# Performance work log

Measured on AMD Instinct MI355X. Metric: run time of the kernel, lower is better.

## Reference

```python
import jax, jax.numpy as jnp
import numpy as np

B, S, E, H, SHARE = 32, 1024, 256, 256, 2


def setup_inputs() -> dict:
    key = jax.random.key(0)
    ks = jax.random.split(key, 14)
    sc_e = 1.0 / np.sqrt(E)
    sc_h = 1.0 / np.sqrt(H)
    mk = lambda k, shape, sc: (jax.random.normal(k, shape, jnp.float32) * sc)
    return {
        "inputs": jax.random.normal(ks[0], (B, S, E), jnp.float32),
        "mask": jnp.ones((B, S), jnp.float32),
        # forward-direction cell params
        "Wx": mk(ks[1], (E, 4 * H), sc_e),
        "Wh": mk(ks[2], (H, 4 * H), sc_h),
        "Ws": mk(ks[3], (H, 4 * H), sc_h),
        "b": jnp.zeros((4 * H,), jnp.float32),
        "Wrx": mk(ks[4], (SHARE, E, H), sc_e),
        "Wrh": mk(ks[5], (SHARE, H, H), sc_h),
        "br": jnp.zeros((SHARE, H), jnp.float32),
        # reverse-direction cell params (deepcopy in torch; distinct draws here)
        "Wx_r": mk(ks[6], (E, 4 * H), sc_e),
        "Wh_r": mk(ks[7], (H, 4 * H), sc_h),
        "Ws_r": mk(ks[8], (H, 4 * H), sc_h),
        "b_r": jnp.zeros((4 * H,), jnp.float32),
        "Wrx_r": mk(ks[9], (SHARE, E, H), sc_e),
        "Wrh_r": mk(ks[10], (SHARE, H, H), sc_h),
        "br_r": jnp.zeros((SHARE, H), jnp.float32),
        "idx": 1,
    }


def _run_dir(xs, ms, params, idx, reverse):
    # xs: [S,B,E] time-major, ms: [S,B]
    Wx, Wh, Ws, b, Wrx, Wrh, br = params
    if reverse:
        xs = xs[::-1]
        ms = ms[::-1]
    Bt = xs.shape[1]
    Hd = Wh.shape[0]
    K = Wrx.shape[0]
    h0 = jnp.zeros((Bt, Hd), xs.dtype)
    c0 = jnp.zeros((Bt, Hd), xs.dtype)
    s0 = jnp.zeros((K, Bt, Hd), xs.dtype)  # shared cells (init_s)

    def step(carry, xm):
        h, c, s = carry
        x_t, m_t = xm
        # gates read x, h, and the idx-selected shared cell
        z = x_t @ Wx + h @ Wh + s[idx] @ Ws + b  # [B, 4H]
        i, f, g, o = jnp.split(z, 4, axis=-1)
        c_new = jax.nn.sigmoid(f) * c + jax.nn.sigmoid(i) * jnp.tanh(g)
        h_new = jax.nn.sigmoid(o) * jnp.tanh(c_new)
        m = m_t[:, None]
        h = m * h_new + (1.0 - m) * h
        c = m * c_new + (1.0 - m) * c
        # shared-cell gates, all K at once: [K,B,H]
        r = jax.nn.sigmoid(
            jnp.einsum("be,keh->kbh", x_t, Wrx)
            + jnp.einsum("bh,khj->kbj", h, Wrh)
            + br[:, None, :]
        )
        s_new = r * s + (1.0 - r) * c[None]
        s = m[None] * s_new + (1.0 - m[None]) * s
        return (h, c, s), (h, c, s)

    _, (hs, cs, ss) = jax.lax.scan(step, (h0, c0, s0), (xs, ms))
    if reverse:
        hs, cs, ss = hs[::-1], cs[::-1], ss[::-1]
    return hs, cs, ss  # [S,B,H], [S,B,H], [S,K,B,H]


def reference(inputs, mask, Wx, Wh, Ws, b, Wrx, Wrh, br,
              Wx_r, Wh_r, Ws_r, b_r, Wrx_r, Wrh_r, br_r, idx):
    xs = inputs.transpose(1, 0, 2)  # [S,B,E]
    ms = mask.T  # [S,B]
    hs_f, cs_f, ss_f = _run_dir(xs, ms, (Wx, Wh, Ws, b, Wrx, Wrh, br), idx, False)
    hs_r, cs_r, ss_r = _run_dir(xs, ms, (Wx_r, Wh_r, Ws_r, b_r, Wrx_r, Wrh_r, br_r), idx, True)
    h_f = jnp.concatenate([hs_f, hs_r], axis=-1)  # [S,B,2H]
    c_f = jnp.concatenate([cs_f, cs_r], axis=-1)  # [S,B,2H]
    # final_list: per shared-cell index, stacked over time -> [K,S,B,2H]
    s_f = jnp.concatenate([ss_f, ss_r], axis=-1).transpose(1, 0, 2, 3)
    return (h_f, c_f, s_f)
```

## Files before the change

### kernel.cpp

```cpp
#include <hip/hip_runtime.h>
#include <hip/hip_bf16.h>
#include <cstdint>
#include <cstddef>


typedef __bf16 bf16x8 __attribute__((ext_vector_type(8)));
typedef float  f32x4  __attribute__((ext_vector_type(4)));

#define DEVINL __device__ __forceinline__

constexpr int Bb = 32, Ss = 1024;
constexpr int NWG = 32;

constexpr size_t OFF_CTR = 0;
constexpr size_t OFF_H   = 1024;
constexpr size_t SZ_HS   = (size_t)2*2*32*256*2;
constexpr size_t OFF_S   = OFF_H + SZ_HS;
constexpr size_t OFF_WX  = OFF_S + SZ_HS;
constexpr size_t SZ_W    = (size_t)2*1024*256*2;
constexpr size_t OFF_WS  = OFF_WX + SZ_W;
constexpr size_t OFF_WRX = OFF_WS + SZ_W;
constexpr size_t SZ_WR   = (size_t)2*2*256*256*2;
constexpr size_t OFF_WRH = OFF_WRX + SZ_WR;

DEVINL unsigned short f2bf(float f) {
    unsigned u = __builtin_bit_cast(unsigned, f);
    u += 0x7FFFu + ((u >> 16) & 1u);
    return (unsigned short)(u >> 16);
}
DEVINL float sigm(float x) { return 1.f / (1.f + __expf(-x)); }

__global__ void prepass(const float* __restrict__ Wx0, const float* __restrict__ Ws0,
                        const float* __restrict__ Wx1, const float* __restrict__ Ws1,
                        const float* __restrict__ Wrx0, const float* __restrict__ Wrh0,
                        const float* __restrict__ Wrx1, const float* __restrict__ Wrh1,
                        unsigned char* __restrict__ ws)
{
    unsigned short* wxT  = (unsigned short*)(ws + OFF_WX);
    unsigned short* wsT  = (unsigned short*)(ws + OFF_WS);
    unsigned short* wrxT = (unsigned short*)(ws + OFF_WRX);
    unsigned short* wrhT = (unsigned short*)(ws + OFF_WRH);
    int tid = blockIdx.x * blockDim.x + threadIdx.x;
    int NT  = gridDim.x * blockDim.x;
    for (int e = tid; e < 2*1024*256; e += NT) {
        int d = e >> 18, r = e & 262143, n = r >> 8, k = r & 255;
        const float* wx = d ? Wx1 : Wx0;
        const float* wz = d ? Ws1 : Ws0;
        wxT[e] = f2bf(wx[k*1024 + n]);
        wsT[e] = f2bf(wz[k*1024 + n]);
    }
    for (int e = tid; e < 2*2*256*256; e += NT) {
        int d = e >> 17, r = e & 131071, kk = r >> 16, r2 = r & 65535;
        int j = r2 >> 8, k = r2 & 255;
        const float* wrx = d ? Wrx1 : Wrx0;
        const float* wrh = d ? Wrh1 : Wrh0;
        wrxT[e] = f2bf(wrx[(kk*256 + k)*256 + j]);
        wrhT[e] = f2bf(wrh[(kk*256 + k)*256 + j]);
    }
    unsigned* z = (unsigned*)(ws + OFF_H);
    for (int e = tid; e < (int)(2*SZ_HS/4); e += NT) z[e] = 0u;
    if (tid < 256) ((unsigned*)ws)[tid] = 0u;
}

__launch_bounds__(256, 1)
__global__ void bislstm(const float* __restrict__ inputs, const float* __restrict__ mask,
                        const float* __restrict__ Wh0, const float* __restrict__ Wh1,
                        const float* __restrict__ b0,  const float* __restrict__ b1,
                        const float* __restrict__ br0, const float* __restrict__ br1,
                        const int* __restrict__ idxp,
                        unsigned char* __restrict__ ws, float* __restrict__ out)
{
    const int bid = blockIdx.x;
    const int d   = bid >> 5;
    const int g   = bid & 31;
    const int tid = threadIdx.x;
    const int wave = tid >> 6, lane = tid & 63;
    const int lm = lane & 15, lq = lane >> 4;

    __shared__ __align__(16) unsigned short sWh[32][264];
    __shared__ __align__(16) unsigned short sA[32][520];
    __shared__ float zs[2][32][16];
    __shared__ float rsx[32][16], rsh[32][16];
    __shared__ float sC[32][8], sH[32][8], sS[2][32][8];
    __shared__ unsigned short sHb[256], sSb[256];

    const float* Whd = d ? Wh1 : Wh0;
    const float* bd  = d ? b1  : b0;
    const float* brd = d ? br1 : br0;
    const unsigned short* wxT  = (const unsigned short*)(ws + OFF_WX)  + (size_t)d*1024*256;
    const unsigned short* wsT  = (const unsigned short*)(ws + OFF_WS)  + (size_t)d*1024*256;
    const unsigned short* wrxT = (const unsigned short*)(ws + OFF_WRX) + (size_t)d*2*256*256;
    const unsigned short* wrhT = (const unsigned short*)(ws + OFF_WRH) + (size_t)d*2*256*256;
    unsigned long long* Hbuf = (unsigned long long*)(ws + OFF_H);
    unsigned long long* Sbuf = (unsigned long long*)(ws + OFF_S);
    unsigned* ctr = (unsigned*)(ws + OFF_CTR) + (size_t)d*64;
    const int idxv = idxp[0];

    for (int i = 0; i < 32; ++i) {
        int e = tid + 256*i, k = e >> 5, nl = e & 31;
        int col = (nl >> 3)*256 + g*8 + (nl & 7);
        sWh[nl][k] = f2bf(Whd[(size_t)k*1024 + col]);
    }
    {
        int b_ = tid >> 3, j = tid & 7;
        sC[b_][j] = 0.f; sH[b_][j] = 0.f; sS[0][b_][j] = 0.f; sS[1][b_][j] = 0.f;
    }
    __syncthreads();

    const int eb = tid >> 3, ej = tid & 7;
    const int gj = g*8 + ej;
    const float bias_i = bd[gj], bias_f = bd[256+gj], bias_g = bd[512+gj], bias_o = bd[768+gj];
    const float brr0 = brd[gj], brr1 = brd[256+gj];

    const int zMt = wave & 1, zNt = wave >> 1;
    const int znl = zNt*16 + lm;
    const int zcol = (znl >> 3)*256 + g*8 + (znl & 7);
    const int rMt = wave & 1;
    const int rks = lm >> 3;
    const int rj  = g*8 + (lm & 7);

    unsigned tgt = 0;
#define GRID_BARRIER()                                                          \
    do {                                                                        \
        __syncthreads();                                                        \
        if (tid == 0) {                                                         \
            __hip_atomic_fetch_add(ctr, 1u, __ATOMIC_RELEASE,                   \
                                   __HIP_MEMORY_SCOPE_AGENT);                   \
            while (__hip_atomic_load(ctr, __ATOMIC_RELAXED,                     \
                                     __HIP_MEMORY_SCOPE_AGENT) < tgt)           \
                __builtin_amdgcn_s_sleep(1);                                    \
            (void)__hip_atomic_load(ctr, __ATOMIC_ACQUIRE,                      \
                                    __HIP_MEMORY_SCOPE_AGENT);                  \
        }                                                                       \
        __syncthreads();                                                        \
    } while (0)

    for (int t = 0; t < Ss; ++t) {
        const int tx = d ? (Ss - 1 - t) : t;
        const int pp = (t + 1) & 1;
        const int pc = t & 1;

        {
            const unsigned long long* hsrc = Hbuf + (size_t)(pp*2 + d)*2048;
            const unsigned long long* ssrc = Sbuf + (size_t)(pp*2 + d)*2048;
#pragma unroll
            for (int i = 0; i < 8; ++i) {
                int e = tid + 256*i;
                int b_ = e >> 6, u4 = e & 63;
                unsigned long long hv = __hip_atomic_load(hsrc + e, __ATOMIC_RELAXED, __HIP_MEMORY_SCOPE_AGENT);
                unsigned long long sv = __hip_atomic_load(ssrc + e, __ATOMIC_RELAXED, __HIP_MEMORY_SCOPE_AGENT);
                *(unsigned long long*)&sA[b_][u4*4]       = hv;
                *(unsigned long long*)&sA[b_][256 + u4*4] = sv;
            }
        }
        __syncthreads();

        f32x4 acc0 = {0.f, 0.f, 0.f, 0.f};
        {
            bf16x8 wsf[8];
#pragma unroll
            for (int kt = 0; kt < 8; ++kt)
                wsf[kt] = *(const bf16x8*)(wsT + (size_t)zcol*256 + 32*kt + 8*lq);
#pragma unroll
            for (int kt = 0; kt < 16; ++kt) {
                bf16x8 a = *(const bf16x8*)&sA[zMt*16 + lm][32*kt + 8*lq];
                bf16x8 bb = (kt < 8) ? *(const bf16x8*)&sWh[znl][32*kt + 8*lq] : wsf[kt - 8];
                acc0 = __builtin_amdgcn_mfma_f32_16x16x32_bf16(a, bb, acc0, 0, 0, 0);
            }
        }
        __syncthreads();

        {
#pragma unroll
            for (int i = 0; i < 8; ++i) {
                int e = tid + 256*i;
                int b_ = e >> 6, c4 = e & 63;
                float4 v = *(const float4*)(inputs + (((size_t)b_*Ss + tx) << 8) + c4*4);
                unsigned long long pk = (unsigned long long)f2bf(v.x)
                                      | ((unsigned long long)f2bf(v.y) << 16)
                                      | ((unsigned long long)f2bf(v.z) << 32)
                                      | ((unsigned long long)f2bf(v.w) << 48);
                *(unsigned long long*)&sA[b_][c4*4] = pk;
            }
        }
        __syncthreads();

        {
            bf16x8 wxf[8];
#pragma unroll
            for (int kt = 0; kt < 8; ++kt)
                wxf[kt] = *(const bf16x8*)(wxT + (size_t)zcol*256 + 32*kt + 8*lq);
#pragma unroll
            for (int kt = 0; kt < 8; ++kt) {
                bf16x8 a = *(const bf16x8*)&sA[zMt*16 + lm][32*kt + 8*lq];
                acc0 = __builtin_amdgcn_mfma_f32_16x16x32_bf16(a, wxf[kt], acc0, 0, 0, 0);
            }
        }
#pragma unroll
        for (int r = 0; r < 4; ++r)
            zs[zNt][zMt*16 + lq*4 + r][lm] = acc0[r];
        __syncthreads();

        float m_, cu_, hu_;
        {
            float zi = zs[0][eb][ej]   + bias_i;
            float zf = zs[0][eb][8+ej] + bias_f;
            float zg = zs[1][eb][ej]   + bias_g;
            float zo = zs[1][eb][8+ej] + bias_o;
            float co = sC[eb][ej], ho = sH[eb][ej];
            float cn = sigm(zf)*co + sigm(zi)*tanhf(zg);
            float hn = sigm(zo)*tanhf(cn);
            m_  = mask[(size_t)eb*Ss + tx];
            cu_ = m_*cn + (1.f - m_)*co;
            hu_ = m_*hn + (1.f - m_)*ho;
            sC[eb][ej] = cu_; sH[eb][ej] = hu_;
            sHb[eb*8 + ej] = f2bf(hu_);
            out[((size_t)tx*32 + eb)*512 + d*256 + gj] = hu_;
            out[16777216 + ((size_t)tx*32 + eb)*512 + d*256 + gj] = cu_;
        }
        __syncthreads();
        if (wave == 0) {
            unsigned long long pk = *(unsigned long long*)&sHb[lane*4];
            int b_ = lane >> 1, half = lane & 1;
            size_t di = (size_t)(pc*2 + d)*2048 + (size_t)b_*64 + g*2 + half;
            __hip_atomic_store(Hbuf + di, pk, __ATOMIC_RELAXED, __HIP_MEMORY_SCOPE_AGENT);
        }
        tgt += NWG; GRID_BARRIER();

        if (wave < 2) {
            f32x4 racc = {0.f, 0.f, 0.f, 0.f};
            bf16x8 wf[8];
#pragma unroll
            for (int kt = 0; kt < 8; ++kt)
                wf[kt] = *(const bf16x8*)(wrxT + (size_t)(rks*256 + rj)*256 + 32*kt + 8*lq);
#pragma unroll
            for (int kt = 0; kt < 8; ++kt) {
                bf16x8 a = *(const bf16x8*)&sA[rMt*16 + lm][32*kt + 8*lq];
                racc = __builtin_amdgcn_mfma_f32_16x16x32_bf16(a, wf[kt], racc, 0, 0, 0);
            }
#pragma unroll
            for (int r = 0; r < 4; ++r)
                rsx[rMt*16 + lq*4 + r][lm] = racc[r];
        }
        __syncthreads();

        {
            const unsigned long long* hsrc = Hbuf + (size_t)(pc*2 + d)*2048;
#pragma unroll
            for (int i = 0; i < 8; ++i) {
                int e = tid + 256*i;
                int b_ = e >> 6, u4 = e & 63;
                unsigned long long hv = __hip_atomic_load(hsrc + e, __ATOMIC_RELAXED, __HIP_MEMORY_SCOPE_AGENT);
                *(unsigned long long*)&sA[b_][256 + u4*4] = hv;
            }
        }
        __syncthreads();

        if (wave >= 2) {
            f32x4 rh = {0.f, 0.f, 0.f, 0.f};
            bf16x8 wf[8];
#pragma unroll
            for (int kt = 0; kt < 8; ++kt)
                wf[kt] = *(const bf16x8*)(wrhT + (size_t)(rks*256 + rj)*256 + 32*kt + 8*lq);
#pragma unroll
            for (int kt = 0; kt < 8; ++kt) {
                bf16x8 a = *(const bf16x8*)&sA[rMt*16 + lm][256 + 32*kt + 8*lq];
                rh = __builtin_amdgcn_mfma_f32_16x16x32_bf16(a, wf[kt], rh, 0, 0, 0);
            }
#pragma unroll
            for (int r = 0; r < 4; ++r)
                rsh[rMt*16 + lq*4 + r][lm] = rh[r];
        }
        __syncthreads();

        {
#pragma unroll
            for (int kk = 0; kk < 2; ++kk) {
                float rv = rsx[eb][kk*8+ej] + rsh[eb][kk*8+ej] + (kk ? brr1 : brr0);
                float rr = sigm(rv);
                float so = sS[kk][eb][ej];
                float sn = rr*so + (1.f - rr)*cu_;
                float su = m_*sn + (1.f - m_)*so;
                sS[kk][eb][ej] = su;
                out[33554432 + (((size_t)kk*1024 + tx)*32 + eb)*512 + d*256 + gj] = su;
                if (kk == idxv) sSb[eb*8 + ej] = f2bf(su);
            }
        }
        __syncthreads();
        if (wave == 0) {
            unsigned long long pk = *(unsigned long long*)&sSb[lane*4];
            int b_ = lane >> 1, half = lane & 1;
            size_t di = (size_t)(pc*2 + d)*2048 + (size_t)b_*64 + g*2 + half;
            __hip_atomic_store(Sbuf + di, pk, __ATOMIC_RELAXED, __HIP_MEMORY_SCOPE_AGENT);
        }
        tgt += NWG; GRID_BARRIER();
    }
#undef GRID_BARRIER
}

extern "C" void kernel_launch(void* const* d_in, const int* in_sizes, int n_in,
                              void* d_out, int out_size, void* d_ws, size_t ws_size,
                              hipStream_t stream) {
    const float* inputs = (const float*)d_in[0];
    const float* mask_  = (const float*)d_in[1];
    const float* Wx0  = (const float*)d_in[2];
    const float* Wh0  = (const float*)d_in[3];
    const float* Ws0  = (const float*)d_in[4];
    const float* b0   = (const float*)d_in[5];
    const float* Wrx0 = (const float*)d_in[6];
    const float* Wrh0 = (const float*)d_in[7];
    const float* br0  = (const float*)d_in[8];
    const float* Wx1  = (const float*)d_in[9];
    const float* Wh1  = (const float*)d_in[10];
    const float* Ws1  = (const float*)d_in[11];
    const float* b1   = (const float*)d_in[12];
    const float* Wrx1 = (const float*)d_in[13];
    const float* Wrh1 = (const float*)d_in[14];
    const float* br1  = (const float*)d_in[15];
    const int*   idxp = (const int*)d_in[16];
    unsigned char* ws = (unsigned char*)d_ws;

    hipLaunchKernelGGL(prepass, dim3(512), dim3(256), 0, stream,
                       Wx0, Ws0, Wx1, Ws1, Wrx0, Wrh0, Wrx1, Wrh1, ws);
    hipLaunchKernelGGL(bislstm, dim3(64), dim3(256), 0, stream,
                       inputs, mask_, Wh0, Wh1, b0, b1, br0, br1, idxp,
                       ws, (float*)d_out);
}
```

Measured before the change: 14.69 ms.

## Replace grid barriers with per-workgroup flags, register-resident weights, prefetch next input

Swaps the counter-based grid barrier for per-workgroup step flags that one wave polls, so each workgroup waits only for data it actually reads. All weight fragments (Wh, Ws, Wx, Wrx/Wrh) are loaded into registers once instead of being re-read from global memory every step. The next timestep's inputs are prefetched into a fragment-ordered shared-memory layout while other waves run, and the per-step sync count drops. This raises register pressure and relies on relaxed atomics plus explicit waitcnt for correctness.

```diff
diff --git a/kernel.cpp b/kernel.cpp
--- a/kernel.cpp
+++ b/kernel.cpp
@@ -6,18 +6,19 @@
 
 typedef __bf16 bf16x8 __attribute__((ext_vector_type(8)));
 typedef float  f32x4  __attribute__((ext_vector_type(4)));
+typedef unsigned long long u64x2 __attribute__((ext_vector_type(2)));
 
 #define DEVINL __device__ __forceinline__
 
-constexpr int Bb = 32, Ss = 1024;
-constexpr int NWG = 32;
-
-constexpr size_t OFF_CTR = 0;
+constexpr int Ss = 1024;
+
+constexpr size_t OFF_FLAGS = 0;
 constexpr size_t OFF_H   = 1024;
-constexpr size_t SZ_HS   = (size_t)2*2*32*256*2;
+constexpr size_t SZ_HS   = (size_t)2*2*32*512;
 constexpr size_t OFF_S   = OFF_H + SZ_HS;
-constexpr size_t OFF_WX  = OFF_S + SZ_HS;
+constexpr size_t OFF_WH  = OFF_S + SZ_HS;
 constexpr size_t SZ_W    = (size_t)2*1024*256*2;
+constexpr size_t OFF_WX  = OFF_WH + SZ_W;
 constexpr size_t OFF_WS  = OFF_WX + SZ_W;
 constexpr size_t OFF_WRX = OFF_WS + SZ_W;
 constexpr size_t SZ_WR   = (size_t)2*2*256*256*2;
@@ -28,14 +29,21 @@
     u += 0x7FFFu + ((u >> 16) & 1u);
     return (unsigned short)(u >> 16);
 }
+DEVINL unsigned long long pack4(float4 v) {
+    return (unsigned long long)f2bf(v.x) | ((unsigned long long)f2bf(v.y) << 16)
+         | ((unsigned long long)f2bf(v.z) << 32) | ((unsigned long long)f2bf(v.w) << 48);
+}
 DEVINL float sigm(float x) { return 1.f / (1.f + __expf(-x)); }
 
-__global__ void prepass(const float* __restrict__ Wx0, const float* __restrict__ Ws0,
-                        const float* __restrict__ Wx1, const float* __restrict__ Ws1,
+__global__ void prepass(const float* __restrict__ Wx0, const float* __restrict__ Wh0,
+                        const float* __restrict__ Ws0,
+                        const float* __restrict__ Wx1, const float* __restrict__ Wh1,
+                        const float* __restrict__ Ws1,
                         const float* __restrict__ Wrx0, const float* __restrict__ Wrh0,
                         const float* __restrict__ Wrx1, const float* __restrict__ Wrh1,
                         unsigned char* __restrict__ ws)
 {
+    unsigned short* whT  = (unsigned short*)(ws + OFF_WH);
     unsigned short* wxT  = (unsigned short*)(ws + OFF_WX);
     unsigned short* wsT  = (unsigned short*)(ws + OFF_WS);
     unsigned short* wrxT = (unsigned short*)(ws + OFF_WRX);
@@ -44,27 +52,24 @@
     int NT  = gridDim.x * blockDim.x;
     for (int e = tid; e < 2*1024*256; e += NT) {
         int d = e >> 18, r = e & 262143, n = r >> 8, k = r & 255;
-        const float* wx = d ? Wx1 : Wx0;
-        const float* wz = d ? Ws1 : Ws0;
-        wxT[e] = f2bf(wx[k*1024 + n]);
-        wsT[e] = f2bf(wz[k*1024 + n]);
+        whT[e] = f2bf((d ? Wh1 : Wh0)[k*1024 + n]);
+        wxT[e] = f2bf((d ? Wx1 : Wx0)[k*1024 + n]);
+        wsT[e] = f2bf((d ? Ws1 : Ws0)[k*1024 + n]);
     }
     for (int e = tid; e < 2*2*256*256; e += NT) {
         int d = e >> 17, r = e & 131071, kk = r >> 16, r2 = r & 65535;
         int j = r2 >> 8, k = r2 & 255;
-        const float* wrx = d ? Wrx1 : Wrx0;
-        const float* wrh = d ? Wrh1 : Wrh0;
-        wrxT[e] = f2bf(wrx[(kk*256 + k)*256 + j]);
-        wrhT[e] = f2bf(wrh[(kk*256 + k)*256 + j]);
-    }
-    unsigned* z = (unsigned*)(ws + OFF_H);
-    for (int e = tid; e < (int)(2*SZ_HS/4); e += NT) z[e] = 0u;
-    if (tid < 256) ((unsigned*)ws)[tid] = 0u;
-}
+        wrxT[e] = f2bf((d ? Wrx1 : Wrx0)[(kk*256 + k)*256 + j]);
+        wrhT[e] = f2bf((d ? Wrh1 : Wrh0)[(kk*256 + k)*256 + j]);
+    }
+    if (blockIdx.x == 0 && threadIdx.x < 256) ((unsigned*)ws)[threadIdx.x] = 0u;
+}
+
+#define FRAG_PTR(Mt,kt,lqv,m) \
+    ((unsigned long long*)(sA + (size_t)(((((Mt)*24+(kt))*4+(lqv))*16+(m))*8)))
 
 __launch_bounds__(256, 1)
 __global__ void bislstm(const float* __restrict__ inputs, const float* __restrict__ mask,
-                        const float* __restrict__ Wh0, const float* __restrict__ Wh1,
                         const float* __restrict__ b0,  const float* __restrict__ b1,
                         const float* __restrict__ br0, const float* __restrict__ br1,
                         const int* __restrict__ idxp,
@@ -77,33 +82,68 @@
     const int wave = tid >> 6, lane = tid & 63;
     const int lm = lane & 15, lq = lane >> 4;
 
-    __shared__ __align__(16) unsigned short sWh[32][264];
-    __shared__ __align__(16) unsigned short sA[32][520];
+    __shared__ __align__(16) unsigned short sA[24576];
     __shared__ float zs[2][32][16];
     __shared__ float rsx[32][16], rsh[32][16];
-    __shared__ float sC[32][8], sH[32][8], sS[2][32][8];
-    __shared__ unsigned short sHb[256], sSb[256];
-
-    const float* Whd = d ? Wh1 : Wh0;
-    const float* bd  = d ? b1  : b0;
-    const float* brd = d ? br1 : br0;
+    __shared__ float sC[32][8], sHs[32][8], sS2[2][32][8];
+    __shared__ __align__(8) unsigned short sHb[256], sSb[256];
+
+    const unsigned short* whT  = (const unsigned short*)(ws + OFF_WH)  + (size_t)d*1024*256;
     const unsigned short* wxT  = (const unsigned short*)(ws + OFF_WX)  + (size_t)d*1024*256;
     const unsigned short* wsT  = (const unsigned short*)(ws + OFF_WS)  + (size_t)d*1024*256;
     const unsigned short* wrxT = (const unsigned short*)(ws + OFF_WRX) + (size_t)d*2*256*256;
     const unsigned short* wrhT = (const unsigned short*)(ws + OFF_WRH) + (size_t)d*2*256*256;
     unsigned long long* Hbuf = (unsigned long long*)(ws + OFF_H);
     unsigned long long* Sbuf = (unsigned long long*)(ws + OFF_S);
-    unsigned* ctr = (unsigned*)(ws + OFF_CTR) + (size_t)d*64;
+    unsigned* flagsH = (unsigned*)ws + d*64;
+    unsigned* flagsS = (unsigned*)ws + 128 + d*64;
     const int idxv = idxp[0];
-
-    for (int i = 0; i < 32; ++i) {
-        int e = tid + 256*i, k = e >> 5, nl = e & 31;
-        int col = (nl >> 3)*256 + g*8 + (nl & 7);
-        sWh[nl][k] = f2bf(Whd[(size_t)k*1024 + col]);
+    const float* bd  = d ? b1  : b0;
+    const float* brd = d ? br1 : br0;
+
+    const int zMt = wave & 1, zNt = wave >> 1;
+    const int znl = zNt*16 + lm;
+    const int zcol = (znl >> 3)*256 + g*8 + (znl & 7);
+    const int rks = lm >> 3;
+    const int rj  = g*8 + (lm & 7);
+
+    bf16x8 whf[8], wsf[8], wxf[8], rwf[8];
+#pragma unroll
+    for (int kt = 0; kt < 8; ++kt) {
+        whf[kt] = *(const bf16x8*)(whT + (size_t)zcol*256 + kt*32 + lq*8);
+        wsf[kt] = *(const bf16x8*)(wsT + (size_t)zcol*256 + kt*32 + lq*8);
+        wxf[kt] = *(const bf16x8*)(wxT + (size_t)zcol*256 + kt*32 + lq*8);
     }
     {
+        const unsigned short* wrT = (wave < 2) ? wrxT : wrhT;
+#pragma unroll
+        for (int kt = 0; kt < 8; ++kt)
+            rwf[kt] = *(const bf16x8*)(wrT + (size_t)(rks*256 + rj)*256 + kt*32 + lq*8);
+    }
+
+    {
+        unsigned long long* z8 = (unsigned long long*)sA;
+#pragma unroll
+        for (int i = 0; i < 16; ++i) {
+            int r = tid + 256*i;
+            int u = (r & 2047) + (r >> 11)*3072;
+            z8[u] = 0ULL;
+        }
         int b_ = tid >> 3, j = tid & 7;
-        sC[b_][j] = 0.f; sH[b_][j] = 0.f; sS[0][b_][j] = 0.f; sS[1][b_][j] = 0.f;
+        sC[b_][j] = 0.f; sHs[b_][j] = 0.f; sS2[0][b_][j] = 0.f; sS2[1][b_][j] = 0.f;
+    }
+    {
+        int tx0 = d ? (Ss - 1) : 0;
+#pragma unroll
+        for (int i = 0; i < 4; ++i) {
+            int b_ = (tid & 7) + 8*i;
+            int j  = tid >> 3;
+            const float* xp = inputs + (((size_t)b_*Ss + tx0) << 8) + j*8;
+            float4 v0 = *(const float4*)xp;
+            float4 v1 = *(const float4*)(xp + 4);
+            u64x2 pk; pk.x = pack4(v0); pk.y = pack4(v1);
+            *(u64x2*)FRAG_PTR(b_ >> 4, 16 + (j >> 2), j & 3, b_ & 15) = pk;
+        }
     }
     __syncthreads();
 
@@ -112,93 +152,26 @@
     const float bias_i = bd[gj], bias_f = bd[256+gj], bias_g = bd[512+gj], bias_o = bd[768+gj];
     const float brr0 = brd[gj], brr1 = brd[256+gj];
 
-    const int zMt = wave & 1, zNt = wave >> 1;
-    const int znl = zNt*16 + lm;
-    const int zcol = (znl >> 3)*256 + g*8 + (znl & 7);
-    const int rMt = wave & 1;
-    const int rks = lm >> 3;
-    const int rj  = g*8 + (lm & 7);
-
-    unsigned tgt = 0;
-#define GRID_BARRIER()                                                          \
-    do {                                                                        \
-        __syncthreads();                                                        \
-        if (tid == 0) {                                                         \
-            __hip_atomic_fetch_add(ctr, 1u, __ATOMIC_RELEASE,                   \
-                                   __HIP_MEMORY_SCOPE_AGENT);                   \
-            while (__hip_atomic_load(ctr, __ATOMIC_RELAXED,                     \
-                                     __HIP_MEMORY_SCOPE_AGENT) < tgt)           \
-                __builtin_amdgcn_s_sleep(1);                                    \
-            (void)__hip_atomic_load(ctr, __ATOMIC_ACQUIRE,                      \
-                                    __HIP_MEMORY_SCOPE_AGENT);                  \
-        }                                                                       \
-        __syncthreads();                                                        \
-    } while (0)
+    const unsigned short* aBase = sA + (size_t)((zMt*96 + lq)*128 + lm*8);
 
     for (int t = 0; t < Ss; ++t) {
         const int tx = d ? (Ss - 1 - t) : t;
-        const int pp = (t + 1) & 1;
         const int pc = t & 1;
-
-        {
-            const unsigned long long* hsrc = Hbuf + (size_t)(pp*2 + d)*2048;
-            const unsigned long long* ssrc = Sbuf + (size_t)(pp*2 + d)*2048;
-#pragma unroll
-            for (int i = 0; i < 8; ++i) {
-                int e = tid + 256*i;
-                int b_ = e >> 6, u4 = e & 63;
-                unsigned long long hv = __hip_atomic_load(hsrc + e, __ATOMIC_RELAXED, __HIP_MEMORY_SCOPE_AGENT);
-                unsigned long long sv = __hip_atomic_load(ssrc + e, __ATOMIC_RELAXED, __HIP_MEMORY_SCOPE_AGENT);
-                *(unsigned long long*)&sA[b_][u4*4]       = hv;
-                *(unsigned long long*)&sA[b_][256 + u4*4] = sv;
-            }
-        }
-        __syncthreads();
-
-        f32x4 acc0 = {0.f, 0.f, 0.f, 0.f};
-        {
-            bf16x8 wsf[8];
-#pragma unroll
-            for (int kt = 0; kt < 8; ++kt)
-                wsf[kt] = *(const bf16x8*)(wsT + (size_t)zcol*256 + 32*kt + 8*lq);
-#pragma unroll
-            for (int kt = 0; kt < 16; ++kt) {
-                bf16x8 a = *(const bf16x8*)&sA[zMt*16 + lm][32*kt + 8*lq];
-                bf16x8 bb = (kt < 8) ? *(const bf16x8*)&sWh[znl][32*kt + 8*lq] : wsf[kt - 8];
-                acc0 = __builtin_amdgcn_mfma_f32_16x16x32_bf16(a, bb, acc0, 0, 0, 0);
-            }
-        }
-        __syncthreads();
-
-        {
-#pragma unroll
-            for (int i = 0; i < 8; ++i) {
-                int e = tid + 256*i;
-                int b_ = e >> 6, c4 = e & 63;
-                float4 v = *(const float4*)(inputs + (((size_t)b_*Ss + tx) << 8) + c4*4);
-                unsigned long long pk = (unsigned long long)f2bf(v.x)
-                                      | ((unsigned long long)f2bf(v.y) << 16)
-                                      | ((unsigned long long)f2bf(v.z) << 32)
-                                      | ((unsigned long long)f2bf(v.w) << 48);
-                *(unsigned long long*)&sA[b_][c4*4] = pk;
-            }
-        }
-        __syncthreads();
-
-        {
-            bf16x8 wxf[8];
-#pragma unroll
-            for (int kt = 0; kt < 8; ++kt)
-                wxf[kt] = *(const bf16x8*)(wxT + (size_t)zcol*256 + 32*kt + 8*lq);
-#pragma unroll
-            for (int kt = 0; kt < 8; ++kt) {
-                bf16x8 a = *(const bf16x8*)&sA[zMt*16 + lm][32*kt + 8*lq];
-                acc0 = __builtin_amdgcn_mfma_f32_16x16x32_bf16(a, wxf[kt], acc0, 0, 0, 0);
-            }
-        }
+        const unsigned want = (unsigned)(t + 1);
+
+        f32x4 acc = {0.f, 0.f, 0.f, 0.f};
+#pragma unroll
+        for (int kt = 0; kt < 8; ++kt)
+            acc = __builtin_amdgcn_mfma_f32_16x16x32_bf16(*(const bf16x8*)(aBase + kt*512), whf[kt], acc, 0, 0, 0);
+#pragma unroll
+        for (int kt = 0; kt < 8; ++kt)
+            acc = __builtin_amdgcn_mfma_f32_16x16x32_bf16(*(const bf16x8*)(aBase + (8+kt)*512), wsf[kt], acc, 0, 0, 0);
+#pragma unroll
+        for (int kt = 0; kt < 8; ++kt)
+            acc = __builtin_amdgcn_mfma_f32_16x16x32_bf16(*(const bf16x8*)(aBase + (16+kt)*512), wxf[kt], acc, 0, 0, 0);
 #pragma unroll
         for (int r = 0; r < 4; ++r)
-            zs[zNt][zMt*16 + lq*4 + r][lm] = acc0[r];
+            zs[zNt][zMt*16 + lq*4 + r][lm] = acc[r];
         __syncthreads();
 
         float m_, cu_, hu_;
@@ -207,69 +180,79 @@
             float zf = zs[0][eb][8+ej] + bias_f;
             float zg = zs[1][eb][ej]   + bias_g;
             float zo = zs[1][eb][8+ej] + bias_o;
-            float co = sC[eb][ej], ho = sH[eb][ej];
+            float co = sC[eb][ej], ho = sHs[eb][ej];
             float cn = sigm(zf)*co + sigm(zi)*tanhf(zg);
             float hn = sigm(zo)*tanhf(cn);
             m_  = mask[(size_t)eb*Ss + tx];
             cu_ = m_*cn + (1.f - m_)*co;
             hu_ = m_*hn + (1.f - m_)*ho;
-            sC[eb][ej] = cu_; sH[eb][ej] = hu_;
-            sHb[eb*8 + ej] = f2bf(hu_);
+            sC[eb][ej] = cu_; sHs[eb][ej] = hu_;
+            sHb[tid] = f2bf(hu_);
             out[((size_t)tx*32 + eb)*512 + d*256 + gj] = hu_;
             out[16777216 + ((size_t)tx*32 + eb)*512 + d*256 + gj] = cu_;
         }
         __syncthreads();
+
         if (wave == 0) {
-            unsigned long long pk = *(unsigned long long*)&sHb[lane*4];
-            int b_ = lane >> 1, half = lane & 1;
-            size_t di = (size_t)(pc*2 + d)*2048 + (size_t)b_*64 + g*2 + half;
-            __hip_atomic_store(Hbuf + di, pk, __ATOMIC_RELAXED, __HIP_MEMORY_SCOPE_AGENT);
-        }
-        tgt += NWG; GRID_BARRIER();
-
+            unsigned long long pk = *(const unsigned long long*)&sHb[lane*4];
+            __hip_atomic_store(Hbuf + (size_t)(pc*2 + d)*2048 + (size_t)(lane>>1)*64 + g*2 + (lane&1),
+                               pk, __ATOMIC_RELAXED, __HIP_MEMORY_SCOPE_AGENT);
+            asm volatile("s_waitcnt vmcnt(0)" ::: "memory");
+            if (lane == 0)
+                __hip_atomic_store(flagsH + g, want, __ATOMIC_RELAXED, __HIP_MEMORY_SCOPE_AGENT);
+        }
         if (wave < 2) {
-            f32x4 racc = {0.f, 0.f, 0.f, 0.f};
-            bf16x8 wf[8];
+            f32x4 ra = {0.f, 0.f, 0.f, 0.f};
 #pragma unroll
             for (int kt = 0; kt < 8; ++kt)
-                wf[kt] = *(const bf16x8*)(wrxT + (size_t)(rks*256 + rj)*256 + 32*kt + 8*lq);
-#pragma unroll
-            for (int kt = 0; kt < 8; ++kt) {
-                bf16x8 a = *(const bf16x8*)&sA[rMt*16 + lm][32*kt + 8*lq];
-                racc = __builtin_amdgcn_mfma_f32_16x16x32_bf16(a, wf[kt], racc, 0, 0, 0);
-            }
+                ra = __builtin_amdgcn_mfma_f32_16x16x32_bf16(*(const bf16x8*)(aBase + (16+kt)*512), rwf[kt], ra, 0, 0, 0);
 #pragma unroll
             for (int r = 0; r < 4; ++r)
-                rsx[rMt*16 + lq*4 + r][lm] = racc[r];
+                rsx[zMt*16 + lq*4 + r][lm] = ra[r];
+        } else if (wave == 3) {
+            for (;;) {
+                unsigned v = __hip_atomic_load(flagsH + (lane & 31), __ATOMIC_RELAXED, __HIP_MEMORY_SCOPE_AGENT);
+                if (__ballot(v < want) == 0ULL) break;
+                __builtin_amdgcn_s_sleep(1);
+            }
+            asm volatile("" ::: "memory");
         }
         __syncthreads();
 
         {
-            const unsigned long long* hsrc = Hbuf + (size_t)(pc*2 + d)*2048;
+            unsigned long long* src = Hbuf + (size_t)(pc*2 + d)*2048;
+#pragma unroll
+            for (int i = 0; i < 4; ++i) {
+                int b_ = (tid & 7) + 8*i;
+                int j  = tid >> 3;
+                unsigned long long v0 = __hip_atomic_load(src + (size_t)b_*64 + j*2,     __ATOMIC_RELAXED, __HIP_MEMORY_SCOPE_AGENT);
+                unsigned long long v1 = __hip_atomic_load(src + (size_t)b_*64 + j*2 + 1, __ATOMIC_RELAXED, __HIP_MEMORY_SCOPE_AGENT);
+                u64x2 pk; pk.x = v0; pk.y = v1;
+                *(u64x2*)FRAG_PTR(b_ >> 4, (j >> 2), j & 3, b_ & 15) = pk;
+            }
+        }
+        __syncthreads();
+
+        if (wave >= 2) {
+            f32x4 ra = {0.f, 0.f, 0.f, 0.f};
+#pragma unroll
+            for (int kt = 0; kt < 8; ++kt)
+                ra = __builtin_amdgcn_mfma_f32_16x16x32_bf16(*(const bf16x8*)(aBase + kt*512), rwf[kt], ra, 0, 0, 0);
+#pragma unroll
+            for (int r = 0; r < 4; ++r)
+                rsh[zMt*16 + lq*4 + r][lm] = ra[r];
+        } else if (t + 1 < Ss) {
+            int txn = d ? (Ss - 2 - t) : (t + 1);
 #pragma unroll
             for (int i = 0; i < 8; ++i) {
-                int e = tid + 256*i;
-                int b_ = e >> 6, u4 = e & 63;
-                unsigned long long hv = __hip_atomic_load(hsrc + e, __ATOMIC_RELAXED, __HIP_MEMORY_SCOPE_AGENT);
-                *(unsigned long long*)&sA[b_][256 + u4*4] = hv;
-            }
-        }
-        __syncthreads();
-
-        if (wave >= 2) {
-            f32x4 rh = {0.f, 0.f, 0.f, 0.f};
-            bf16x8 wf[8];
-#pragma unroll
-            for (int kt = 0; kt < 8; ++kt)
-                wf[kt] = *(const bf16x8*)(wrhT + (size_t)(rks*256 + rj)*256 + 32*kt + 8*lq);
-#pragma unroll
-            for (int kt = 0; kt < 8; ++kt) {
-                bf16x8 a = *(const bf16x8*)&sA[rMt*16 + lm][256 + 32*kt + 8*lq];
-                rh = __builtin_amdgcn_mfma_f32_16x16x32_bf16(a, wf[kt], rh, 0, 0, 0);
-            }
-#pragma unroll
-            for (int r = 0; r < 4; ++r)
-                rsh[rMt*16 + lq*4 + r][lm] = rh[r];
+                int b_ = (tid & 7) + 8*(i >> 1);
+                int j  = (tid >> 3) + 16*(i & 1);
+                const float* xp = inputs + (((size_t)b_*Ss + txn) << 8) + j*8;
+                float4 v0 = *(const float4*)xp;
+                float4 v1 = *(const float4*)(xp + 4);
+                u64x2 pk; pk.x = pack4(v0); pk.y = pack4(v1);
+                *(u64x2*)FRAG_PTR(b_ >> 4, 16 + (j >> 2), j & 3, b_ & 15) = pk;
+            }
         }
         __syncthreads();
 
@@ -278,24 +261,47 @@
             for (int kk = 0; kk < 2; ++kk) {
                 float rv = rsx[eb][kk*8+ej] + rsh[eb][kk*8+ej] + (kk ? brr1 : brr0);
                 float rr = sigm(rv);
-                float so = sS[kk][eb][ej];
+                float so = sS2[kk][eb][ej];
                 float sn = rr*so + (1.f - rr)*cu_;
                 float su = m_*sn + (1.f - m_)*so;
-                sS[kk][eb][ej] = su;
+                sS2[kk][eb][ej] = su;
                 out[33554432 + (((size_t)kk*1024 + tx)*32 + eb)*512 + d*256 + gj] = su;
-                if (kk == idxv) sSb[eb*8 + ej] = f2bf(su);
-            }
-        }
-        __syncthreads();
+                if (kk == idxv) sSb[tid] = f2bf(su);
+            }
+        }
+        __syncthreads();
+
         if (wave == 0) {
-            unsigned long long pk = *(unsigned long long*)&sSb[lane*4];
-            int b_ = lane >> 1, half = lane & 1;
-            size_t di = (size_t)(pc*2 + d)*2048 + (size_t)b_*64 + g*2 + half;
-            __hip_atomic_store(Sbuf + di, pk, __ATOMIC_RELAXED, __HIP_MEMORY_SCOPE_AGENT);
-        }
-        tgt += NWG; GRID_BARRIER();
-    }
-#undef GRID_BARRIER
+            unsigned long long pk = *(const unsigned long long*)&sSb[lane*4];
+            __hip_atomic_store(Sbuf + (size_t)(pc*2 + d)*2048 + (size_t)(lane>>1)*64 + g*2 + (lane&1),
+                               pk, __ATOMIC_RELAXED, __HIP_MEMORY_SCOPE_AGENT);
+            asm volatile("s_waitcnt vmcnt(0)" ::: "memory");
+            if (lane == 0)
+                __hip_atomic_store(flagsS + g, want, __ATOMIC_RELAXED, __HIP_MEMORY_SCOPE_AGENT);
+        } else if (wave == 3 && t + 1 < Ss) {
+            for (;;) {
+                unsigned v = __hip_atomic_load(flagsS + (lane & 31), __ATOMIC_RELAXED, __HIP_MEMORY_SCOPE_AGENT);
+                if (__ballot(v < want) == 0ULL) break;
+                __builtin_amdgcn_s_sleep(1);
+            }
+            asm volatile("" ::: "memory");
+        }
+        __syncthreads();
+
+        if (t + 1 < Ss) {
+            unsigned long long* src = Sbuf + (size_t)(pc*2 + d)*2048;
+#pragma unroll
+            for (int i = 0; i < 4; ++i) {
+                int b_ = (tid & 7) + 8*i;
+                int j  = tid >> 3;
+                unsigned long long v0 = __hip_atomic_load(src + (size_t)b_*64 + j*2,     __ATOMIC_RELAXED, __HIP_MEMORY_SCOPE_AGENT);
+                unsigned long long v1 = __hip_atomic_load(src + (size_t)b_*64 + j*2 + 1, __ATOMIC_RELAXED, __HIP_MEMORY_SCOPE_AGENT);
+                u64x2 pk; pk.x = v0; pk.y = v1;
+                *(u64x2*)FRAG_PTR(b_ >> 4, 8 + (j >> 2), j & 3, b_ & 15) = pk;
+            }
+            __syncthreads();
+        }
+    }
 }
 
 extern "C" void kernel_launch(void* const* d_in, const int* in_sizes, int n_in,
@@ -321,8 +327,8 @@
     unsigned char* ws = (unsigned char*)d_ws;
 
     hipLaunchKernelGGL(prepass, dim3(512), dim3(256), 0, stream,
-                       Wx0, Ws0, Wx1, Ws1, Wrx0, Wrh0, Wrx1, Wrh1, ws);
+                       Wx0, Wh0, Ws0, Wx1, Wh1, Ws1, Wrx0, Wrh0, Wrx1, Wrh1, ws);
     hipLaunchKernelGGL(bislstm, dim3(64), dim3(256), 0, stream,
-                       inputs, mask_, Wh0, Wh1, b0, b1, br0, br1, idxp,
+                       inputs, mask_, b0, b1, br0, br1, idxp,
                        ws, (float*)d_out);
 }
```

Result: faster. 11.99 ms (-18.3%).
